# Optimization experiments

Hardware: AMD Instinct MI355X
Metric: run time of the kernel (lower is better)

The kernel has to match this reference:

```python
import jax, jax.numpy as jnp
import numpy as np

B, N, D, H = 128, 197, 384, 1536  # batch, patches+CLS, embed_dim, hidden_dim


def _layer_norm(x, g, b, eps=1e-5):
    m = jnp.mean(x, axis=-1, keepdims=True)
    v = jnp.mean(jnp.square(x - m), axis=-1, keepdims=True)
    return (x - m) * jax.lax.rsqrt(v + eps) * g + b


def setup_inputs() -> dict:
    key = jax.random.key(0)
    ks = jax.random.split(key, 8)
    x = jax.random.normal(ks[0], (B, N, D), dtype=jnp.float32)
    # quantum circuit surrogates: orthogonal-style square matrices
    V = jax.random.normal(ks[1], (D, D), dtype=jnp.float32) / np.sqrt(D)
    W = jax.random.normal(ks[2], (D, D), dtype=jnp.float32) / np.sqrt(D)
    ln1_g = jnp.ones((D,), jnp.float32); ln1_b = jnp.zeros((D,), jnp.float32)
    ln2_g = jnp.ones((D,), jnp.float32); ln2_b = jnp.zeros((D,), jnp.float32)
    W1 = jax.random.normal(ks[3], (D, H), dtype=jnp.float32) / np.sqrt(D)
    b1 = jnp.zeros((H,), jnp.float32)
    W2 = jax.random.normal(ks[4], (H, D), dtype=jnp.float32) / np.sqrt(H)
    b2 = jnp.zeros((D,), jnp.float32)
    return {"x": x, "ln1_g": ln1_g, "ln1_b": ln1_b, "V": V, "W": W,
            "ln2_g": ln2_g, "ln2_b": ln2_b, "W1": W1, "b1": b1, "W2": W2, "b2": b2}


def reference(x, ln1_g, ln1_b, V, W, ln2_g, ln2_b, W1, b1, W2, b2):
    inp = _layer_norm(x, ln1_g, ln1_b)
    # normalization across the patch axis (dim=1), exactly as in the torch code
    inp = inp / jnp.sqrt(jnp.sum(jnp.square(inp) + 1e-4, axis=1, keepdims=True) + 1e-8)
    # Vx circuit: unary-basis probabilities |(V x_i)_d|^2 -> vx[b, d, i]
    vx = jnp.square(jnp.einsum('de,bne->bdn', V, inp))            # [B, D, N]
    # xWx circuit: (x_i^T W x_j)^2 -> xwx[b, i, j]
    y = jnp.einsum('bnd,de->bne', inp, W)                         # [B, N, D]
    xwx = jnp.square(jnp.einsum('bne,bme->bnm', y, inp))          # [B, N, N]
    vx = jnp.sqrt(vx + 1e-8)
    xwx = jnp.sqrt(xwx + 1e-8)
    attn = jax.nn.softmax(xwx, axis=-1)                           # [B, N, N]
    t = jnp.einsum('bnm,bdm->bnd', attn, vx)                      # attn @ vx^T
    x = x + t
    h = _layer_norm(x, ln2_g, ln2_b)
    h = jax.nn.gelu(h @ W1 + b1) @ W2 + b2                        # dropout=0 (eval)
    return x + h
```

## Files before the change

### kernel.cpp

```cpp
#include <hip/hip_runtime.h>
#include <math.h>

typedef unsigned short u16;
typedef unsigned int u32;
typedef __bf16 bfv8 __attribute__((ext_vector_type(8)));
typedef float f32x4 __attribute__((ext_vector_type(4)));

#define BB 128
#define NN 197
#define DD 384
#define HH 1536
#define BN (BB*NN)
#define NP 224

__device__ __forceinline__ u16 f2bf(float x){ u32 u; __builtin_memcpy(&u,&x,4); u = (u + 0x7fffu + ((u>>16)&1u))>>16; return (u16)u; }

__device__ __forceinline__ float fast_gelu(float z){
  float t2 = 1.5957691216f*z*(1.f + 0.044715f*z*z);
  return z * __builtin_amdgcn_rcpf(1.f + __expf(-t2));
}

__device__ __forceinline__ void gload16(const void* g, void* s){
  __builtin_amdgcn_global_load_lds(
      (const __attribute__((address_space(1))) void*)g,
      (__attribute__((address_space(3))) void*)s, 16, 0, 0);
}

__global__ __launch_bounds__(256) void ln1_stats(const float* __restrict__ x,
    float* __restrict__ mu, float* __restrict__ rv){
  int row = blockIdx.x*4 + (threadIdx.x>>6);
  int lane = threadIdx.x & 63;
  const float* xr = x + (long)row*DD;
  float s=0.f, ss=0.f;
  #pragma unroll
  for (int j=0;j<DD/64;j++){ float v = xr[lane + j*64]; s+=v; ss+=v*v; }
  #pragma unroll
  for (int m=32;m;m>>=1){ s += __shfl_xor(s,m); ss += __shfl_xor(ss,m); }
  if (lane==0){
    float mn = s*(1.f/DD);
    float var = ss*(1.f/DD) - mn*mn;
    mu[row]=mn; rv[row]=1.f/sqrtf(var+1e-5f);
  }
}

__global__ __launch_bounds__(256) void colnorm(const float* __restrict__ x,
    const float* __restrict__ mu, const float* __restrict__ rv,
    const float* __restrict__ g, const float* __restrict__ bt,
    float* __restrict__ scale){
  int i = blockIdx.x*256 + threadIdx.x;
  int b = i/DD, d = i - b*DD;
  const float* xp = x + (long)b*NN*DD + d;
  float gd = g[d], bd = bt[d];
  float s = 0.f;
  for (int n=0;n<NN;n++){
    float v = (xp[(long)n*DD] - mu[b*NN+n]) * rv[b*NN+n] * gd + bd;
    s += v*v;
  }
  scale[i] = 1.f/sqrtf(s + 197.f*1e-4f + 1e-8f);
}

__global__ __launch_bounds__(256) void ln_apply(const float* __restrict__ x,
    const float* __restrict__ mu, const float* __restrict__ rv,
    const float* __restrict__ g, const float* __restrict__ bt,
    const float* __restrict__ scale, u16* __restrict__ inpn){
  long i = (long)blockIdx.x*256 + threadIdx.x;
  int d = (int)(i % DD);
  long row = i / DD;
  int b = (int)(row / NN);
  float v = (x[i]-mu[row])*rv[row]*g[d]+bt[d];
  inpn[i] = f2bf(v * scale[b*DD+d]);
}

__global__ __launch_bounds__(256) void prep_weights(const float* __restrict__ V, const float* __restrict__ W,
    const float* __restrict__ W1, const float* __restrict__ W2,
    u16* __restrict__ Vb, u16* __restrict__ Wt, u16* __restrict__ W1t, u16* __restrict__ W2t){
  int i = blockIdx.x*256 + threadIdx.x;
  if (i < DD*DD){
    Vb[i] = f2bf(V[i]);
    int r = i/DD, c = i - r*DD;
    Wt[c*DD + r] = f2bf(W[i]);
  }
  {
    int r = i/HH, c = i - r*HH;
    W1t[(long)c*DD + r] = f2bf(W1[i]);
    int r2 = i/DD, c2 = i - r2*DD;
    W2t[(long)c2*HH + r2] = f2bf(W2[i]);
  }
}

__global__ __launch_bounds__(256) void softmax_rows(const float* __restrict__ S, u16* __restrict__ attn){
  int row = blockIdx.x*4 + (threadIdx.x>>6);
  int lane = threadIdx.x & 63;
  const float* sr = S + (long)row*NP;
  float v[4]; float mx = -1e30f;
  #pragma unroll
  for (int j=0;j<4;j++){ int c = lane + j*64; v[j] = (c<NN)? sr[c] : -1e30f; mx = fmaxf(mx, v[j]); }
  #pragma unroll
  for (int m=32;m;m>>=1) mx = fmaxf(mx, __shfl_xor(mx,m));
  float sm = 0.f;
  #pragma unroll
  for (int j=0;j<4;j++){ v[j] = __expf(v[j]-mx); sm += v[j]; }
  #pragma unroll
  for (int m=32;m;m>>=1) sm += __shfl_xor(sm,m);
  float inv = __builtin_amdgcn_rcpf(sm);
  u16* ar = attn + (long)row*NP;
  #pragma unroll
  for (int j=0;j<4;j++){ int c = lane + j*64; if (c<NP) ar[c] = f2bf(v[j]*inv); }
}

__global__ __launch_bounds__(256) void ln2_fused(const float* __restrict__ x2,
    const float* __restrict__ g, const float* __restrict__ bt, u16* __restrict__ h){
  int row = blockIdx.x*4 + (threadIdx.x>>6);
  int lane = threadIdx.x & 63;
  const float* xr = x2 + (long)row*DD;
  float v[6]; float s=0.f, ss=0.f;
  #pragma unroll
  for (int j=0;j<6;j++){ v[j]=xr[lane+j*64]; s+=v[j]; ss+=v[j]*v[j]; }
  #pragma unroll
  for (int m=32;m;m>>=1){ s+=__shfl_xor(s,m); ss+=__shfl_xor(ss,m); }
  float mn = s*(1.f/DD);
  float rvv = 1.f/sqrtf(ss*(1.f/DD)-mn*mn+1e-5f);
  u16* hr = h + (long)row*DD;
  #pragma unroll
  for (int j=0;j<6;j++){ int d = lane+j*64; hr[d] = f2bf((v[j]-mn)*rvv*g[d]+bt[d]); }
}

struct EpiUt { u16* ut;
  __device__ void operator()(int, int r0, int c, const f32x4* col, int mf) const {
    for (int m=0;m<mf;m++)
      #pragma unroll
      for (int i=0;i<4;i++){
        int r = r0 + m*16 + i;
        int b = r/NN, p = r - b*NN;
        float v = col[m][i];
        ut[((long)b*DD + c)*NP + p] = f2bf(sqrtf(v*v + 1e-8f));
      }
  }};
struct EpiY { u16* y;
  __device__ void operator()(int, int r0, int c, const f32x4* col, int mf) const {
    u16* yp = y + (long)r0*DD + c;
    for (int m=0;m<mf;m++)
      #pragma unroll
      for (int i=0;i<4;i++)
        yp[(long)(m*16+i)*DD] = f2bf(col[m][i]);
  }};
struct EpiS { float* s;
  __device__ void operator()(int b, int r0, int c, const f32x4* col, int mf) const {
    float* sp = s + ((long)b*NN + r0)*NP + c;
    for (int m=0;m<mf;m++)
      #pragma unroll
      for (int i=0;i<4;i++){
        int r = r0 + m*16 + i;
        float v = col[m][i];
        if (r < NN) sp[(long)(m*16+i)*NP] = sqrtf(v*v + 1e-8f);
      }
  }};
struct EpiX2 { float* x2; const float* x;
  __device__ void operator()(int b, int r0, int c, const f32x4* col, int mf) const {
    long base = ((long)b*NN + r0)*DD + c;
    for (int m=0;m<mf;m++)
      #pragma unroll
      for (int i=0;i<4;i++){
        int r = r0 + m*16 + i;
        if (r < NN){ long idx = base + (long)(m*16+i)*DD; x2[idx] = x[idx] + col[m][i]; }
      }
  }};
struct EpiGelu { u16* g; const float* b1;
  __device__ void operator()(int, int r0, int c, const f32x4* col, int mf) const {
    float bb = b1[c];
    u16* gp = g + (long)r0*HH + c;
    for (int m=0;m<mf;m++)
      #pragma unroll
      for (int i=0;i<4;i++)
        gp[(long)(m*16+i)*HH] = f2bf(fast_gelu(col[m][i] + bb));
  }};
struct EpiOut { float* o; const float* x2; const float* b2;
  __device__ void operator()(int, int r0, int c, const f32x4* col, int mf) const {
    float bb = b2[c];
    long base = (long)r0*DD + c;
    for (int m=0;m<mf;m++)
      #pragma unroll
      for (int i=0;i<4;i++){
        long idx = base + (long)(m*16+i)*DD;
        o[idx] = x2[idx] + col[m][i] + bb;
      }
  }};

template<int BM, class Epi>
__global__ __launch_bounds__(256) void gemm_nt(const u16* __restrict__ A, const u16* __restrict__ B,
    int M, int N, int K, int lda, int ldb, long sA, long sB, int NT, Epi epi)
{
  constexpr int MF = BM/32;
  constexpr int ALOADS = BM/64;
  __shared__ __align__(16) u16 As[2][BM*32];
  __shared__ __align__(16) u16 Bs[2][128*32];
  int wg;
  { int flat = blockIdx.x, nwg = gridDim.x;
    int xcd = flat & 7, local = flat >> 3;
    int q = nwg >> 3, r = nwg & 7;
    wg = (xcd < r ? xcd*(q+1) : r*(q+1) + (xcd-r)*q) + local; }
  const int bm = wg / NT, bn = wg - bm*NT;
  const int bat = blockIdx.y;
  const u16* Ab = A + (long)bat*sA;
  const u16* Bb = B + (long)bat*sB;
  const int t = threadIdx.x, lane = t&63, wid = t>>6, wr = wid>>1, wc = wid&1;
  const int row0 = bm*BM, col0 = bn*128;

  long aoff[ALOADS]; int asoff[ALOADS];
  #pragma unroll
  for (int i=0;i<ALOADS;i++){
    int ob = (i*256+t)*16;
    int r = ob>>6, ke = (ob&63)>>1;
    int ra = row0+r; if (ra>M-1) ra=M-1;
    aoff[i] = (long)ra*lda + ke; asoff[i] = ob;
  }
  long boff[2]; int bsoff[2];
  #pragma unroll
  for (int i=0;i<2;i++){
    int ob = (i*256+t)*16;
    int r = ob>>6, ke = (ob&63)>>1;
    int rb = col0+r; if (rb>N-1) rb=N-1;
    boff[i] = (long)rb*ldb + ke; bsoff[i] = ob;
  }

  auto stage = [&](int buf, int k0){
    #pragma unroll
    for (int i=0;i<ALOADS;i++) gload16(Ab + aoff[i] + k0, (char*)As[buf] + asoff[i]);
    #pragma unroll
    for (int i=0;i<2;i++)      gload16(Bb + boff[i] + k0, (char*)Bs[buf] + bsoff[i]);
  };

  f32x4 acc[MF][4] = {};
  const int kg = (lane>>4)*8, rl = lane&15;
  const int ntile = K/32;

  stage(0, 0);
  stage(1, 32);
  int buf = 0;
  for (int tt=0; tt<ntile; ++tt){
    if (tt+1 < ntile){
      if constexpr (ALOADS == 1) asm volatile("s_waitcnt vmcnt(3)" ::: "memory");
      else                       asm volatile("s_waitcnt vmcnt(4)" ::: "memory");
    } else {
      asm volatile("s_waitcnt vmcnt(0)" ::: "memory");
    }
    __builtin_amdgcn_sched_barrier(0);
    __builtin_amdgcn_s_barrier();

    bfv8 af[MF], bfr[4];
    #pragma unroll
    for (int m=0;m<MF;m++) af[m]  = *(const bfv8*)&As[buf][(wr*(BM/2) + m*16 + rl)*32 + kg];
    #pragma unroll
    for (int n=0;n<4;n++)  bfr[n] = *(const bfv8*)&Bs[buf][(wc*64 + n*16 + rl)*32 + kg];
    #pragma unroll
    for (int m=0;m<MF;m++)
      #pragma unroll
      for (int n=0;n<4;n++)
        acc[m][n] = __builtin_amdgcn_mfma_f32_16x16x32_bf16(af[m], bfr[n], acc[m][n], 0,0,0);

    __builtin_amdgcn_s_barrier();
    __builtin_amdgcn_sched_barrier(0);
    if (tt+2 < ntile) stage(buf, (tt+2)*32);
    buf ^= 1;
  }

  const int rbase = row0 + wr*(BM/2) + (lane>>4)*4;
  const int cbase = col0 + wc*64 + rl;
  #pragma unroll
  for (int n=0;n<4;n++){
    int c = cbase + n*16;
    if (c < N){
      f32x4 colv[MF];
      #pragma unroll
      for (int m=0;m<MF;m++) colv[m] = acc[m][n];
      epi(bat, rbase, c, colv, MF);
    }
  }
}

extern "C" void kernel_launch(void* const* d_in, const int* in_sizes, int n_in,
                              void* d_out, int out_size, void* d_ws, size_t ws_size,
                              hipStream_t stream){
  const float* x     = (const float*)d_in[0];
  const float* g1    = (const float*)d_in[1];
  const float* b1n   = (const float*)d_in[2];
  const float* V     = (const float*)d_in[3];
  const float* W     = (const float*)d_in[4];
  const float* g2    = (const float*)d_in[5];
  const float* b2n   = (const float*)d_in[6];
  const float* W1    = (const float*)d_in[7];
  const float* bias1 = (const float*)d_in[8];
  const float* W2    = (const float*)d_in[9];
  const float* bias2 = (const float*)d_in[10];
  float* out = (float*)d_out;

  char* ws = (char*)d_ws;
  size_t off = 0;
  auto take = [&](size_t bytes)->char*{ char* p = ws + off; off += (bytes + 255) & ~(size_t)255; return p; };

  float* mu    = (float*)take((size_t)BN*4);
  float* rv    = (float*)take((size_t)BN*4);
  float* scale = (float*)take((size_t)BB*DD*4);
  char* aliasBase = ws + off;
  u16*  inpn = (u16*) take((size_t)BN*DD*2);
  u16*  Ut   = (u16*) take((size_t)BB*DD*NP*2);
  u16*  Yb   = (u16*) take((size_t)BN*DD*2);
  float* S   = (float*)take((size_t)BN*NP*4);
  u16*  attn = (u16*) take((size_t)BN*NP*2);
  float* x2  = (float*)take((size_t)BN*DD*4);
  u16*  h    = (u16*) take((size_t)BN*DD*2);
  u16*  Vb   = (u16*) take((size_t)DD*DD*2);
  u16*  Wt   = (u16*) take((size_t)DD*DD*2);
  u16*  W1t  = (u16*) take((size_t)DD*HH*2);
  u16*  W2t  = (u16*) take((size_t)DD*HH*2);
  u16*  G    = (u16*)aliasBase;

  prep_weights<<<DD*HH/256, 256, 0, stream>>>(V, W, W1, W2, Vb, Wt, W1t, W2t);
  ln1_stats  <<<BN/4,       256, 0, stream>>>(x, mu, rv);
  colnorm    <<<BB*DD/256,  256, 0, stream>>>(x, mu, rv, g1, b1n, scale);
  ln_apply   <<<BN*DD/256,  256, 0, stream>>>(x, mu, rv, g1, b1n, scale, inpn);
  (void)hipMemsetAsync(Ut, 0, (size_t)BB*DD*NP*2, stream);

  { dim3 grid(394*3, 1);
    gemm_nt<64,EpiUt><<<grid,256,0,stream>>>(inpn, Vb, BN, DD, DD, DD, DD, 0, 0, 3, EpiUt{Ut}); }
  { dim3 grid(394*3, 1);
    gemm_nt<64,EpiY><<<grid,256,0,stream>>>(inpn, Wt, BN, DD, DD, DD, DD, 0, 0, 3, EpiY{Yb}); }
  { dim3 grid(4*2, BB);
    gemm_nt<64,EpiS><<<grid,256,0,stream>>>(Yb, inpn, NN, NN, DD, DD, DD,
                                         (long)NN*DD, (long)NN*DD, 2, EpiS{S}); }
  softmax_rows<<<BN/4, 256, 0, stream>>>(S, attn);
  { dim3 grid(4*3, BB);
    gemm_nt<64,EpiX2><<<grid,256,0,stream>>>(attn, Ut, NN, DD, NP, NP, NP,
                                          (long)NN*NP, (long)DD*NP, 3, EpiX2{x2, x}); }
  ln2_fused<<<BN/4, 256, 0, stream>>>(x2, g2, b2n, h);
  { dim3 grid(197*12, 1);
    gemm_nt<128,EpiGelu><<<grid,256,0,stream>>>(h, W1t, BN, HH, DD, DD, DD, 0, 0, 12, EpiGelu{G, bias1}); }
  { dim3 grid(394*3, 1);
    gemm_nt<64,EpiOut><<<grid,256,0,stream>>>(G, W2t, BN, DD, HH, HH, HH, 0, 0, 3, EpiOut{out, x2, bias2}); }
}
```

Measured before the change: 423.1 us.

## Deepen GEMM LDS pipeline to multi-stage and swizzle LDS layout

```diff
diff --git a/kernel.cpp b/kernel.cpp
--- a/kernel.cpp
+++ b/kernel.cpp
@@ -186,14 +186,16 @@
       }
   }};
 
-template<int BM, class Epi>
+#define WAITV(N) asm volatile("s_waitcnt vmcnt(" #N ")" ::: "memory")
+template<int BM, int D, class Epi>
 __global__ __launch_bounds__(256) void gemm_nt(const u16* __restrict__ A, const u16* __restrict__ B,
     int M, int N, int K, int lda, int ldb, long sA, long sB, int NT, Epi epi)
 {
   constexpr int MF = BM/32;
   constexpr int ALOADS = BM/64;
-  __shared__ __align__(16) u16 As[2][BM*32];
-  __shared__ __align__(16) u16 Bs[2][128*32];
+  constexpr int L = ALOADS + 2;
+  __shared__ __align__(16) u16 As[D][BM*32];
+  __shared__ __align__(16) u16 Bs[D][128*32];
   int wg;
   { int flat = blockIdx.x, nwg = gridDim.x;
     int xcd = flat & 7, local = flat >> 3;
@@ -210,17 +212,19 @@
   #pragma unroll
   for (int i=0;i<ALOADS;i++){
     int ob = (i*256+t)*16;
-    int r = ob>>6, ke = (ob&63)>>1;
+    int r = ob>>6;
+    int sg = ((ob>>4)&3) ^ (r&3) ^ ((r>>2)&3);
     int ra = row0+r; if (ra>M-1) ra=M-1;
-    aoff[i] = (long)ra*lda + ke; asoff[i] = ob;
+    aoff[i] = (long)ra*lda + sg*8; asoff[i] = ob;
   }
   long boff[2]; int bsoff[2];
   #pragma unroll
   for (int i=0;i<2;i++){
     int ob = (i*256+t)*16;
-    int r = ob>>6, ke = (ob&63)>>1;
+    int r = ob>>6;
+    int sg = ((ob>>4)&3) ^ (r&3) ^ ((r>>2)&3);
     int rb = col0+r; if (rb>N-1) rb=N-1;
-    boff[i] = (long)rb*ldb + ke; bsoff[i] = ob;
+    boff[i] = (long)rb*ldb + sg*8; bsoff[i] = ob;
   }
 
   auto stage = [&](int buf, int k0){
@@ -231,27 +235,39 @@
   };
 
   f32x4 acc[MF][4] = {};
-  const int kg = (lane>>4)*8, rl = lane&15;
+  const int rl = lane&15, kslot = lane>>4;
   const int ntile = K/32;
 
-  stage(0, 0);
-  stage(1, 32);
-  int buf = 0;
+  #pragma unroll
+  for (int p=0;p<D-1;p++) if (p < ntile) stage(p, p*32);
+
   for (int tt=0; tt<ntile; ++tt){
-    if (tt+1 < ntile){
-      if constexpr (ALOADS == 1) asm volatile("s_waitcnt vmcnt(3)" ::: "memory");
-      else                       asm volatile("s_waitcnt vmcnt(4)" ::: "memory");
-    } else {
-      asm volatile("s_waitcnt vmcnt(0)" ::: "memory");
+    const int buf = tt % D;
+    {
+      int rem = ntile - 1 - tt;
+      int nf = rem < D-2 ? rem : D-2;
+      if constexpr (L==3){
+        if (nf>=2) WAITV(6); else if (nf==1) WAITV(3); else WAITV(0);
+      } else {
+        if (nf>=2) WAITV(8); else if (nf==1) WAITV(4); else WAITV(0);
+      }
     }
     __builtin_amdgcn_sched_barrier(0);
     __builtin_amdgcn_s_barrier();
 
     bfv8 af[MF], bfr[4];
     #pragma unroll
-    for (int m=0;m<MF;m++) af[m]  = *(const bfv8*)&As[buf][(wr*(BM/2) + m*16 + rl)*32 + kg];
-    #pragma unroll
-    for (int n=0;n<4;n++)  bfr[n] = *(const bfv8*)&Bs[buf][(wc*64 + n*16 + rl)*32 + kg];
+    for (int m=0;m<MF;m++){
+      int rowA = wr*(BM/2) + m*16 + rl;
+      int sl = kslot ^ (rowA&3) ^ ((rowA>>2)&3);
+      af[m] = *(const bfv8*)((const char*)As[buf] + rowA*64 + sl*16);
+    }
+    #pragma unroll
+    for (int n=0;n<4;n++){
+      int rowB = wc*64 + n*16 + rl;
+      int sl = kslot ^ (rowB&3) ^ ((rowB>>2)&3);
+      bfr[n] = *(const bfv8*)((const char*)Bs[buf] + rowB*64 + sl*16);
+    }
     #pragma unroll
     for (int m=0;m<MF;m++)
       #pragma unroll
@@ -260,8 +276,7 @@
 
     __builtin_amdgcn_s_barrier();
     __builtin_amdgcn_sched_barrier(0);
-    if (tt+2 < ntile) stage(buf, (tt+2)*32);
-    buf ^= 1;
+    if (tt+D-1 < ntile) stage((tt+D-1)%D, (tt+D-1)*32);
   }
 
   const int rbase = row0 + wr*(BM/2) + (lane>>4)*4;
@@ -322,19 +337,19 @@
   (void)hipMemsetAsync(Ut, 0, (size_t)BB*DD*NP*2, stream);
 
   { dim3 grid(394*3, 1);
-    gemm_nt<64,EpiUt><<<grid,256,0,stream>>>(inpn, Vb, BN, DD, DD, DD, DD, 0, 0, 3, EpiUt{Ut}); }
+    gemm_nt<64,4,EpiUt><<<grid,256,0,stream>>>(inpn, Vb, BN, DD, DD, DD, DD, 0, 0, 3, EpiUt{Ut}); }
   { dim3 grid(394*3, 1);
-    gemm_nt<64,EpiY><<<grid,256,0,stream>>>(inpn, Wt, BN, DD, DD, DD, DD, 0, 0, 3, EpiY{Yb}); }
+    gemm_nt<64,4,EpiY><<<grid,256,0,stream>>>(inpn, Wt, BN, DD, DD, DD, DD, 0, 0, 3, EpiY{Yb}); }
   { dim3 grid(4*2, BB);
-    gemm_nt<64,EpiS><<<grid,256,0,stream>>>(Yb, inpn, NN, NN, DD, DD, DD,
+    gemm_nt<64,4,EpiS><<<grid,256,0,stream>>>(Yb, inpn, NN, NN, DD, DD, DD,
                                          (long)NN*DD, (long)NN*DD, 2, EpiS{S}); }
   softmax_rows<<<BN/4, 256, 0, stream>>>(S, attn);
   { dim3 grid(4*3, BB);
-    gemm_nt<64,EpiX2><<<grid,256,0,stream>>>(attn, Ut, NN, DD, NP, NP, NP,
+    gemm_nt<64,4,EpiX2><<<grid,256,0,stream>>>(attn, Ut, NN, DD, NP, NP, NP,
                                           (long)NN*NP, (long)DD*NP, 3, EpiX2{x2, x}); }
   ln2_fused<<<BN/4, 256, 0, stream>>>(x2, g2, b2n, h);
   { dim3 grid(197*12, 1);
-    gemm_nt<128,EpiGelu><<<grid,256,0,stream>>>(h, W1t, BN, HH, DD, DD, DD, 0, 0, 12, EpiGelu{G, bias1}); }
+    gemm_nt<128,3,EpiGelu><<<grid,256,0,stream>>>(h, W1t, BN, HH, DD, DD, DD, 0, 0, 12, EpiGelu{G, bias1}); }
   { dim3 grid(394*3, 1);
-    gemm_nt<64,EpiOut><<<grid,256,0,stream>>>(G, W2t, BN, DD, HH, HH, HH, 0, 0, 3, EpiOut{out, x2, bias2}); }
-}
+    gemm_nt<64,4,EpiOut><<<grid,256,0,stream>>>(G, W2t, BN, DD, HH, HH, HH, 0, 0, 3, EpiOut{out, x2, bias2}); }
+}
```

Measured after the change: 435.3 us. 1.03x slower.

## Fuse V and W projections into one GEMM, store intermediates in bf16

Applied to the files above, without the earlier changes.

```diff
diff --git a/kernel.cpp b/kernel.cpp
--- a/kernel.cpp
+++ b/kernel.cpp
@@ -13,6 +13,7 @@
 #define BN (BB*NN)
 #define NP 224
 
+__device__ __forceinline__ float bf2f(u16 h){ u32 u = ((u32)h)<<16; float f; __builtin_memcpy(&f,&u,4); return f; }
 __device__ __forceinline__ u16 f2bf(float x){ u32 u; __builtin_memcpy(&u,&x,4); u = (u + 0x7fffu + ((u>>16)&1u))>>16; return (u16)u; }
 
 __device__ __forceinline__ float fast_gelu(float z){
@@ -25,6 +26,8 @@
       (const __attribute__((address_space(1))) void*)g,
       (__attribute__((address_space(3))) void*)s, 16, 0, 0);
 }
+
+#define WAITV(N) asm volatile("s_waitcnt vmcnt(" #N ")" ::: "memory")
 
 __global__ __launch_bounds__(256) void ln1_stats(const float* __restrict__ x,
     float* __restrict__ mu, float* __restrict__ rv){
@@ -88,13 +91,34 @@
   }
 }
 
-__global__ __launch_bounds__(256) void softmax_rows(const float* __restrict__ S, u16* __restrict__ attn){
+__global__ __launch_bounds__(256) void transpose_pad(const u16* __restrict__ U, u16* __restrict__ Ut){
+  __shared__ u16 tile[32][33];
+  int b = blockIdx.x, dt = blockIdx.y, pt = blockIdx.z;
+  int tx = threadIdx.x & 31, ty = threadIdx.x >> 5;
+  const u16* Ub = U + (long)b*NN*DD;
+  #pragma unroll
+  for (int j=0;j<4;j++){
+    int p = pt*32 + ty + j*8;
+    int d = dt*32 + tx;
+    tile[ty+j*8][tx] = (p<NN) ? Ub[(long)p*DD + d] : (u16)0;
+  }
+  __syncthreads();
+  u16* Utb = Ut + (long)b*DD*NP;
+  #pragma unroll
+  for (int j=0;j<4;j++){
+    int d = dt*32 + ty + j*8;
+    int p = pt*32 + tx;
+    Utb[(long)d*NP + p] = tile[tx][ty+j*8];
+  }
+}
+
+__global__ __launch_bounds__(256) void softmax_rows(const u16* __restrict__ S, u16* __restrict__ attn){
   int row = blockIdx.x*4 + (threadIdx.x>>6);
   int lane = threadIdx.x & 63;
-  const float* sr = S + (long)row*NP;
+  const u16* sr = S + (long)row*NP;
   float v[4]; float mx = -1e30f;
   #pragma unroll
-  for (int j=0;j<4;j++){ int c = lane + j*64; v[j] = (c<NN)? sr[c] : -1e30f; mx = fmaxf(mx, v[j]); }
+  for (int j=0;j<4;j++){ int c = lane + j*64; v[j] = (c<NN)? bf2f(sr[c]) : -1e30f; mx = fmaxf(mx, v[j]); }
   #pragma unroll
   for (int m=32;m;m>>=1) mx = fmaxf(mx, __shfl_xor(mx,m));
   float sm = 0.f;
@@ -108,14 +132,14 @@
   for (int j=0;j<4;j++){ int c = lane + j*64; if (c<NP) ar[c] = f2bf(v[j]*inv); }
 }
 
-__global__ __launch_bounds__(256) void ln2_fused(const float* __restrict__ x2,
+__global__ __launch_bounds__(256) void ln2_fused(const u16* __restrict__ x2,
     const float* __restrict__ g, const float* __restrict__ bt, u16* __restrict__ h){
   int row = blockIdx.x*4 + (threadIdx.x>>6);
   int lane = threadIdx.x & 63;
-  const float* xr = x2 + (long)row*DD;
+  const u16* xr = x2 + (long)row*DD;
   float v[6]; float s=0.f, ss=0.f;
   #pragma unroll
-  for (int j=0;j<6;j++){ v[j]=xr[lane+j*64]; s+=v[j]; ss+=v[j]*v[j]; }
+  for (int j=0;j<6;j++){ v[j]=bf2f(xr[lane+j*64]); s+=v[j]; ss+=v[j]*v[j]; }
   #pragma unroll
   for (int m=32;m;m>>=1){ s+=__shfl_xor(s,m); ss+=__shfl_xor(ss,m); }
   float mn = s*(1.f/DD);
@@ -125,44 +149,25 @@
   for (int j=0;j<6;j++){ int d = lane+j*64; hr[d] = f2bf((v[j]-mn)*rvv*g[d]+bt[d]); }
 }
 
-struct EpiUt { u16* ut;
-  __device__ void operator()(int, int r0, int c, const f32x4* col, int mf) const {
-    for (int m=0;m<mf;m++)
-      #pragma unroll
-      for (int i=0;i<4;i++){
-        int r = r0 + m*16 + i;
-        int b = r/NN, p = r - b*NN;
-        float v = col[m][i];
-        ut[((long)b*DD + c)*NP + p] = f2bf(sqrtf(v*v + 1e-8f));
-      }
-  }};
-struct EpiY { u16* y;
-  __device__ void operator()(int, int r0, int c, const f32x4* col, int mf) const {
-    u16* yp = y + (long)r0*DD + c;
-    for (int m=0;m<mf;m++)
-      #pragma unroll
-      for (int i=0;i<4;i++)
-        yp[(long)(m*16+i)*DD] = f2bf(col[m][i]);
-  }};
-struct EpiS { float* s;
+struct EpiS { u16* s;
   __device__ void operator()(int b, int r0, int c, const f32x4* col, int mf) const {
-    float* sp = s + ((long)b*NN + r0)*NP + c;
+    u16* sp = s + ((long)b*NN + r0)*NP + c;
     for (int m=0;m<mf;m++)
       #pragma unroll
       for (int i=0;i<4;i++){
         int r = r0 + m*16 + i;
         float v = col[m][i];
-        if (r < NN) sp[(long)(m*16+i)*NP] = sqrtf(v*v + 1e-8f);
+        if (r < NN) sp[(long)(m*16+i)*NP] = f2bf(sqrtf(v*v + 1e-8f));
       }
   }};
-struct EpiX2 { float* x2; const float* x;
+struct EpiX2 { u16* x2; const float* x;
   __device__ void operator()(int b, int r0, int c, const f32x4* col, int mf) const {
     long base = ((long)b*NN + r0)*DD + c;
     for (int m=0;m<mf;m++)
       #pragma unroll
       for (int i=0;i<4;i++){
         int r = r0 + m*16 + i;
-        if (r < NN){ long idx = base + (long)(m*16+i)*DD; x2[idx] = x[idx] + col[m][i]; }
+        if (r < NN){ long idx = base + (long)(m*16+i)*DD; x2[idx] = f2bf(x[idx] + col[m][i]); }
       }
   }};
 struct EpiGelu { u16* g; const float* b1;
@@ -174,7 +179,7 @@
       for (int i=0;i<4;i++)
         gp[(long)(m*16+i)*HH] = f2bf(fast_gelu(col[m][i] + bb));
   }};
-struct EpiOut { float* o; const float* x2; const float* b2;
+struct EpiOut { float* o; const u16* x2; const float* b2;
   __device__ void operator()(int, int r0, int c, const f32x4* col, int mf) const {
     float bb = b2[c];
     long base = (long)r0*DD + c;
@@ -182,7 +187,7 @@
       #pragma unroll
       for (int i=0;i<4;i++){
         long idx = base + (long)(m*16+i)*DD;
-        o[idx] = x2[idx] + col[m][i] + bb;
+        o[idx] = bf2f(x2[idx]) + col[m][i] + bb;
       }
   }};
 
@@ -239,10 +244,9 @@
   int buf = 0;
   for (int tt=0; tt<ntile; ++tt){
     if (tt+1 < ntile){
-      if constexpr (ALOADS == 1) asm volatile("s_waitcnt vmcnt(3)" ::: "memory");
-      else                       asm volatile("s_waitcnt vmcnt(4)" ::: "memory");
+      if constexpr (ALOADS == 1) WAITV(3); else WAITV(4);
     } else {
-      asm volatile("s_waitcnt vmcnt(0)" ::: "memory");
+      WAITV(0);
     }
     __builtin_amdgcn_sched_barrier(0);
     __builtin_amdgcn_s_barrier();
@@ -275,6 +279,91 @@
       for (int m=0;m<MF;m++) colv[m] = acc[m][n];
       epi(bat, rbase, c, colv, MF);
     }
+  }
+}
+
+__global__ __launch_bounds__(256) void gemm12(const u16* __restrict__ A,
+    const u16* __restrict__ B1, const u16* __restrict__ B2,
+    u16* __restrict__ U, u16* __restrict__ Y)
+{
+  __shared__ __align__(16) u16 As[2][64*32];
+  __shared__ __align__(16) u16 B1s[2][128*32];
+  __shared__ __align__(16) u16 B2s[2][128*32];
+  int wg;
+  { int flat = blockIdx.x, nwg = gridDim.x;
+    int xcd = flat & 7, local = flat >> 3;
+    int q = nwg >> 3, r = nwg & 7;
+    wg = (xcd < r ? xcd*(q+1) : r*(q+1) + (xcd-r)*q) + local; }
+  const int bm = wg/3, bn = wg - bm*3;
+  const int t = threadIdx.x, lane = t&63, wid = t>>6, wr = wid>>1, wc = wid&1;
+  const int row0 = bm*64, col0 = bn*128;
+
+  int ob = t*16, r = ob>>6, ke = (ob&63)>>1;
+  long aoff = (long)(row0+r)*DD + ke;
+  int asoff = ob;
+  long boff[2]; int bsoff[2];
+  #pragma unroll
+  for (int i=0;i<2;i++){
+    int ob2 = (i*256+t)*16, r2 = ob2>>6, ke2 = (ob2&63)>>1;
+    boff[i] = (long)(col0+r2)*DD + ke2; bsoff[i] = ob2;
+  }
+
+  auto stage = [&](int buf, int k0){
+    gload16(A + aoff + k0, (char*)As[buf] + asoff);
+    #pragma unroll
+    for (int i=0;i<2;i++){
+      gload16(B1 + boff[i] + k0, (char*)B1s[buf] + bsoff[i]);
+      gload16(B2 + boff[i] + k0, (char*)B2s[buf] + bsoff[i]);
+    }
+  };
+
+  f32x4 acc1[2][4] = {}, acc2[2][4] = {};
+  const int kg = (lane>>4)*8, rl = lane&15;
+
+  stage(0, 0);
+  stage(1, 32);
+  int buf = 0;
+  for (int tt=0; tt<12; ++tt){
+    if (tt < 11) WAITV(5); else WAITV(0);
+    __builtin_amdgcn_sched_barrier(0);
+    __builtin_amdgcn_s_barrier();
+
+    bfv8 af[2], b1r[4], b2r[4];
+    #pragma unroll
+    for (int m=0;m<2;m++) af[m] = *(const bfv8*)&As[buf][(wr*32 + m*16 + rl)*32 + kg];
+    #pragma unroll
+    for (int n=0;n<4;n++){
+      b1r[n] = *(const bfv8*)&B1s[buf][(wc*64 + n*16 + rl)*32 + kg];
+      b2r[n] = *(const bfv8*)&B2s[buf][(wc*64 + n*16 + rl)*32 + kg];
+    }
+    #pragma unroll
+    for (int m=0;m<2;m++)
+      #pragma unroll
+      for (int n=0;n<4;n++){
+        acc1[m][n] = __builtin_amdgcn_mfma_f32_16x16x32_bf16(af[m], b1r[n], acc1[m][n], 0,0,0);
+        acc2[m][n] = __builtin_amdgcn_mfma_f32_16x16x32_bf16(af[m], b2r[n], acc2[m][n], 0,0,0);
+      }
+
+    __builtin_amdgcn_s_barrier();
+    __builtin_amdgcn_sched_barrier(0);
+    if (tt+2 < 12) stage(buf, (tt+2)*32);
+    buf ^= 1;
+  }
+
+  const int rbase = row0 + wr*32 + (lane>>4)*4;
+  const int cbase = col0 + wc*64 + rl;
+  #pragma unroll
+  for (int n=0;n<4;n++){
+    int c = cbase + n*16;
+    #pragma unroll
+    for (int m=0;m<2;m++)
+      #pragma unroll
+      for (int i=0;i<4;i++){
+        long idx = (long)(rbase + m*16 + i)*DD + c;
+        float v1 = acc1[m][n][i];
+        U[idx] = f2bf(sqrtf(v1*v1 + 1e-8f));
+        Y[idx] = f2bf(acc2[m][n][i]);
+      }
   }
 }
 
@@ -303,11 +392,12 @@
   float* scale = (float*)take((size_t)BB*DD*4);
   char* aliasBase = ws + off;
   u16*  inpn = (u16*) take((size_t)BN*DD*2);
+  u16*  U    = (u16*) take((size_t)BN*DD*2);
   u16*  Ut   = (u16*) take((size_t)BB*DD*NP*2);
   u16*  Yb   = (u16*) take((size_t)BN*DD*2);
-  float* S   = (float*)take((size_t)BN*NP*4);
+  u16*  S    = (u16*) take((size_t)BN*NP*2);
   u16*  attn = (u16*) take((size_t)BN*NP*2);
-  float* x2  = (float*)take((size_t)BN*DD*4);
+  u16*  x2   = (u16*) take((size_t)BN*DD*2);
   u16*  h    = (u16*) take((size_t)BN*DD*2);
   u16*  Vb   = (u16*) take((size_t)DD*DD*2);
   u16*  Wt   = (u16*) take((size_t)DD*DD*2);
@@ -319,12 +409,10 @@
   ln1_stats  <<<BN/4,       256, 0, stream>>>(x, mu, rv);
   colnorm    <<<BB*DD/256,  256, 0, stream>>>(x, mu, rv, g1, b1n, scale);
   ln_apply   <<<BN*DD/256,  256, 0, stream>>>(x, mu, rv, g1, b1n, scale, inpn);
-  (void)hipMemsetAsync(Ut, 0, (size_t)BB*DD*NP*2, stream);
-
-  { dim3 grid(394*3, 1);
-    gemm_nt<64,EpiUt><<<grid,256,0,stream>>>(inpn, Vb, BN, DD, DD, DD, DD, 0, 0, 3, EpiUt{Ut}); }
-  { dim3 grid(394*3, 1);
-    gemm_nt<64,EpiY><<<grid,256,0,stream>>>(inpn, Wt, BN, DD, DD, DD, DD, 0, 0, 3, EpiY{Yb}); }
+
+  gemm12<<<394*3, 256, 0, stream>>>(inpn, Vb, Wt, U, Yb);
+  { dim3 grid(BB, DD/32, NP/32);
+    transpose_pad<<<grid, 256, 0, stream>>>(U, Ut); }
   { dim3 grid(4*2, BB);
     gemm_nt<64,EpiS><<<grid,256,0,stream>>>(Yb, inpn, NN, NN, DD, DD, DD,
                                          (long)NN*DD, (long)NN*DD, 2, EpiS{S}); }
```

New measurement: 395.1 us. 6.6% less time.
